# Optimization experiments

Measured on AMD Instinct MI355X. Metric: run time of the kernel, lower is better.

Reference implementation:

```python
import jax, jax.numpy as jnp
import numpy as np

NEG_SLOPE = 0.2
EPS = 1e-12


def setup_inputs() -> dict:
    key = jax.random.key(0)
    k1, k2, k3, k4, k5 = jax.random.split(key, 5)
    N, E, IN, OUT = 100000, 1600000, 256, 64
    x = jax.random.normal(k1, (N, IN), dtype=jnp.float32)
    edge_index = jax.random.randint(k2, (2, E), 0, N, dtype=jnp.int64)
    # GATConv (heads=1) parameters: lin weight, att_src, att_dst, bias
    W = jax.random.normal(k3, (IN, OUT), dtype=jnp.float32) * (1.0 / np.sqrt(IN))
    att_src = jax.random.normal(k4, (OUT,), dtype=jnp.float32) * (1.0 / np.sqrt(OUT))
    att_dst = jax.random.normal(k5, (OUT,), dtype=jnp.float32) * (1.0 / np.sqrt(OUT))
    bias = jnp.zeros((OUT,), dtype=jnp.float32)
    return {"x": x, "edge_index": edge_index, "W": W,
            "att_src": att_src, "att_dst": att_dst, "bias": bias}


def reference(x, edge_index, W, att_src, att_dst, bias):
    N = x.shape[0]
    # PyG GATConv default add_self_loops=True
    loops = jnp.arange(N, dtype=edge_index.dtype)
    src = jnp.concatenate([edge_index[0], loops])  # source j of edge (j -> i)
    dst = jnp.concatenate([edge_index[1], loops])  # target i (softmax segment)

    h = x @ W                                      # [N, out]
    a_src = h @ att_src                            # [N] per-node source score
    a_dst = h @ att_dst                            # [N] per-node target score

    e = jax.nn.leaky_relu(a_src[src] + a_dst[dst], NEG_SLOPE)  # [E+N]
    # segment softmax over incoming edges of each destination node
    e_max = jax.ops.segment_max(e, dst, num_segments=N)
    e = jnp.exp(e - e_max[dst])
    denom = jax.ops.segment_sum(e, dst, num_segments=N)
    alpha = e / denom[dst]                         # [E+N]

    # scatter-aggregate: out[i] = sum_j alpha_ij * h[j]
    out = jax.ops.segment_sum(alpha[:, None] * h[src], dst, num_segments=N)
    out = out + bias

    # dropout (p=0.3) in eval mode is identity; then F.normalize (row-wise L2)
    nrm = jnp.sqrt(jnp.sum(out * out, axis=-1, keepdims=True))
    return out / jnp.maximum(nrm, EPS)
```

## Files before the change

### kernel.cpp

```cpp
#include <hip/hip_runtime.h>
#include <hip/hip_bf16.h>
#include <math.h>

#define NEG_SLOPE 0.2f
#define EPS_NRM 1e-12f
#define K_IN 256
#define C_OUT 64
#define BK 32
#define TILE_M 64
#define XPAD 36

__global__ __launch_bounds__(256) void gemm_att(
    const float* __restrict__ x, const float* __restrict__ W,
    const float* __restrict__ att_s, const float* __restrict__ att_d,
    __hip_bfloat16* __restrict__ h, float* __restrict__ a_src_arr,
    float* __restrict__ a_dst_arr, int N,
    const int* __restrict__ dstA, int* __restrict__ cnt, int E)
{
    __shared__ float xs[2][TILE_M][XPAD];
    __shared__ float ws[2][BK][C_OUT];

    int t  = threadIdx.x;
    int tx = t & 15;
    int ty = t >> 4;
    int row0 = blockIdx.x * TILE_M;

    int xr  = t >> 2;
    int xko = (t & 3) * 8;
    int srow = row0 + xr; if (srow >= N) srow = N - 1;
    const float* xp = x + (size_t)srow * K_IN + xko;

    int wkr = t >> 3;
    int wco = (t & 7) * 8;
    const float* wp = W + (size_t)wkr * C_OUT + wco;

    float acc[4][4];
#pragma unroll
    for (int r = 0; r < 4; ++r)
#pragma unroll
        for (int c = 0; c < 4; ++c) acc[r][c] = 0.f;

    float4 xA = *(const float4*)(xp);
    float4 xB = *(const float4*)(xp + 4);
    float4 wA = *(const float4*)(wp);
    float4 wB = *(const float4*)(wp + 4);
    *(float4*)&xs[0][xr][xko]       = xA;
    *(float4*)&xs[0][xr][xko + 4]   = xB;
    *(float4*)&ws[0][wkr][wco]      = wA;
    *(float4*)&ws[0][wkr][wco + 4]  = wB;
    __syncthreads();

    int buf = 0;
    for (int k0 = 0; k0 < K_IN; k0 += BK) {
        const bool more = (k0 + BK) < K_IN;
        if (more) {
            xA = *(const float4*)(xp + k0 + BK);
            xB = *(const float4*)(xp + k0 + BK + 4);
            wA = *(const float4*)(wp + (size_t)(k0 + BK) * C_OUT);
            wB = *(const float4*)(wp + (size_t)(k0 + BK) * C_OUT + 4);
        }

#pragma unroll
        for (int kk = 0; kk < BK; kk += 4) {
            float xq[4][4];
            *(float4*)xq[0] = *(const float4*)&xs[buf][ty * 4 + 0][kk];
            *(float4*)xq[1] = *(const float4*)&xs[buf][ty * 4 + 1][kk];
            *(float4*)xq[2] = *(const float4*)&xs[buf][ty * 4 + 2][kk];
            *(float4*)xq[3] = *(const float4*)&xs[buf][ty * 4 + 3][kk];
#pragma unroll
            for (int j = 0; j < 4; ++j) {
                float4 wv = *(const float4*)&ws[buf][kk + j][tx * 4];
#pragma unroll
                for (int r = 0; r < 4; ++r) {
                    acc[r][0] += xq[r][j] * wv.x;
                    acc[r][1] += xq[r][j] * wv.y;
                    acc[r][2] += xq[r][j] * wv.z;
                    acc[r][3] += xq[r][j] * wv.w;
                }
            }
        }

        if (more) {
            *(float4*)&xs[buf ^ 1][xr][xko]      = xA;
            *(float4*)&xs[buf ^ 1][xr][xko + 4]  = xB;
            *(float4*)&ws[buf ^ 1][wkr][wco]     = wA;
            *(float4*)&ws[buf ^ 1][wkr][wco + 4] = wB;
            __syncthreads();
            buf ^= 1;
        }
    }

    float4 avl = *(const float4*)(att_s + tx * 4);
    float4 dvl = *(const float4*)(att_d + tx * 4);
#pragma unroll
    for (int r = 0; r < 4; ++r) {
        int row = row0 + ty * 4 + r;
        float ps = acc[r][0] * avl.x + acc[r][1] * avl.y +
                   acc[r][2] * avl.z + acc[r][3] * avl.w;
        float pd = acc[r][0] * dvl.x + acc[r][1] * dvl.y +
                   acc[r][2] * dvl.z + acc[r][3] * dvl.w;
#pragma unroll
        for (int d = 1; d < 16; d <<= 1) {
            ps += __shfl_xor(ps, d, 64);
            pd += __shfl_xor(pd, d, 64);
        }
        if (row < N) {
            if (tx == 0) { a_src_arr[row] = ps; a_dst_arr[row] = pd; }
            __hip_bfloat16 hb[4];
#pragma unroll
            for (int c = 0; c < 4; ++c) hb[c] = __float2bfloat16(acc[r][c]);
            *(ushort2*)(h + (size_t)row * C_OUT + tx * 4) =
                make_ushort2(*(unsigned short*)&hb[0], *(unsigned short*)&hb[1]);
            *(ushort2*)(h + (size_t)row * C_OUT + tx * 4 + 2) =
                make_ushort2(*(unsigned short*)&hb[2], *(unsigned short*)&hb[3]);
        }
    }

    int stride = gridDim.x * blockDim.x;
    for (int i = blockIdx.x * blockDim.x + t; i < E; i += stride)
        atomicAdd(&cnt[dstA[i]], 1);
}

__global__ __launch_bounds__(256) void scan_p1(
    const int* __restrict__ cnt, int* __restrict__ partials, int n)
{
    int b = blockIdx.x, t = threadIdx.x;
    int base = b * 1024;
    int s = 0;
#pragma unroll
    for (int j = 0; j < 4; ++j) {
        int i = base + t * 4 + j;
        if (i < n) s += cnt[i];
    }
    for (int d = 1; d < 64; d <<= 1) s += __shfl_xor(s, d, 64);
    __shared__ int wsum[4];
    int lane = t & 63, wid = t >> 6;
    if (lane == 0) wsum[wid] = s;
    __syncthreads();
    if (t == 0) partials[b] = wsum[0] + wsum[1] + wsum[2] + wsum[3];
}

__global__ __launch_bounds__(256) void scan_p2(int* partials, int nb)
{
    __shared__ int buf[256];
    int t = threadIdx.x;
    int v = (t < nb) ? partials[t] : 0;
    buf[t] = v;
    __syncthreads();
    for (int d = 1; d < 256; d <<= 1) {
        int w = (t >= d) ? buf[t - d] : 0;
        __syncthreads();
        buf[t] += w;
        __syncthreads();
    }
    if (t < nb) partials[t] = buf[t] - v;
}

__global__ __launch_bounds__(256) void scan_p3(
    const int* __restrict__ cnt, const int* __restrict__ partials,
    int* __restrict__ offsets, int n)
{
    int b = blockIdx.x, t = threadIdx.x;
    int base = b * 1024;
    int v[4];
    int s = 0;
#pragma unroll
    for (int j = 0; j < 4; ++j) {
        int i = base + t * 4 + j;
        v[j] = (i < n) ? cnt[i] : 0;
        s += v[j];
    }
    int lane = t & 63, wid = t >> 6;
    int incl = s;
    for (int d = 1; d < 64; d <<= 1) {
        int w = __shfl_up(incl, d, 64);
        if (lane >= d) incl += w;
    }
    __shared__ int wsum[4];
    __shared__ int wbase[4];
    if (lane == 63) wsum[wid] = incl;
    __syncthreads();
    if (t == 0) {
        int r = 0;
        for (int i = 0; i < 4; ++i) { wbase[i] = r; r += wsum[i]; }
    }
    __syncthreads();
    int run = partials[b] + wbase[wid] + (incl - s);
#pragma unroll
    for (int j = 0; j < 4; ++j) {
        int i = base + t * 4 + j;
        if (i < n) {
            offsets[i] = run;
            run += v[j];
            if (i == n - 1) offsets[n] = run;
        }
    }
}

__global__ __launch_bounds__(256) void scatter_edges(
    const int* __restrict__ srcA, const int* __restrict__ dstA,
    const int* __restrict__ offsets, int* __restrict__ cursor,
    const float* __restrict__ a_src, const float* __restrict__ a_dst,
    unsigned long long* __restrict__ csr, int E)
{
    int i = blockIdx.x * blockDim.x + threadIdx.x;
    if (i >= E) return;
    int s = srcA[i], d = dstA[i];
    float e = a_src[s] + a_dst[d];
    e = fmaxf(e, NEG_SLOPE * e);
    float w = __expf(e);
    int pos = offsets[d] + atomicAdd(&cursor[d], 1);
    unsigned long long packed =
        (unsigned long long)(unsigned)s |
        ((unsigned long long)__float_as_uint(w) << 32);
    __builtin_nontemporal_store(packed, &csr[pos]);
}

__global__ __launch_bounds__(256) void gat_pull(
    const int* __restrict__ offsets, const int2* __restrict__ csr,
    const unsigned short* __restrict__ h, const float* __restrict__ a_src,
    const float* __restrict__ a_dst, const float* __restrict__ bias,
    float* __restrict__ out, int N)
{
    int gw   = (blockIdx.x * blockDim.x + threadIdx.x) >> 6;
    int lane = threadIdx.x & 63;
    int grp  = lane >> 4;
    int gl   = lane & 15;
    int node = gw * 4 + grp;
    bool valid = node < N;
    int nv = valid ? node : 0;

    int beg = offsets[nv];
    int n   = valid ? (offsets[nv + 1] - beg) : 0;
    const int2* ce = csr + (n ? beg : 0);

    float asv = a_src[nv], adv = a_dst[nv];
    float es = asv + adv; es = fmaxf(es, NEG_SLOPE * es);
    float ws = __expf(es);
    unsigned long long hu = *(const unsigned long long*)
        (h + (size_t)nv * C_OUT + 4 * gl);
    unsigned hl = (unsigned)hu, hh = (unsigned)(hu >> 32);
    float acc0 = ws * __uint_as_float(hl << 16);
    float acc1 = ws * __uint_as_float(hl & 0xffff0000u);
    float acc2 = ws * __uint_as_float(hh << 16);
    float acc3 = ws * __uint_as_float(hh & 0xffff0000u);
    float den = ws;

    int2 c0 = ce[0];
    int2 c1 = ce[(n > 1) ? 1 : 0];
    unsigned long long u0 = *(const unsigned long long*)
        (h + (size_t)c0.x * C_OUT + 4 * gl);
    unsigned long long u1 = *(const unsigned long long*)
        (h + (size_t)c1.x * C_OUT + 4 * gl);

    for (int p = 0; p < n; p += 2) {
        int2 m0 = ce[(p + 2 < n) ? p + 2 : 0];
        int2 m1 = ce[(p + 3 < n) ? p + 3 : 0];
        unsigned long long v0 = *(const unsigned long long*)
            (h + (size_t)m0.x * C_OUT + 4 * gl);
        unsigned long long v1 = *(const unsigned long long*)
            (h + (size_t)m1.x * C_OUT + 4 * gl);

        float w0 = __int_as_float(c0.y);
        float w1 = (p + 1 < n) ? __int_as_float(c1.y) : 0.f;
        unsigned l0 = (unsigned)u0, h0 = (unsigned)(u0 >> 32);
        unsigned l1 = (unsigned)u1, h1 = (unsigned)(u1 >> 32);
        den  += w0 + w1;
        acc0 += w0 * __uint_as_float(l0 << 16)
              + w1 * __uint_as_float(l1 << 16);
        acc1 += w0 * __uint_as_float(l0 & 0xffff0000u)
              + w1 * __uint_as_float(l1 & 0xffff0000u);
        acc2 += w0 * __uint_as_float(h0 << 16)
              + w1 * __uint_as_float(h1 << 16);
        acc3 += w0 * __uint_as_float(h0 & 0xffff0000u)
              + w1 * __uint_as_float(h1 & 0xffff0000u);

        c0 = m0; c1 = m1; u0 = v0; u1 = v1;
    }

    float4 bl = *(const float4*)(bias + 4 * gl);
    float rd = 1.f / den;
    float o0 = acc0 * rd + bl.x;
    float o1 = acc1 * rd + bl.y;
    float o2 = acc2 * rd + bl.z;
    float o3 = acc3 * rd + bl.w;

    float sq = o0 * o0 + o1 * o1 + o2 * o2 + o3 * o3;
#pragma unroll
    for (int d = 1; d < 16; d <<= 1) sq += __shfl_xor(sq, d, 64);
    float rn = 1.f / fmaxf(sqrtf(sq), EPS_NRM);

    if (valid)
        *(float4*)(out + (size_t)node * C_OUT + 4 * gl) =
            make_float4(o0 * rn, o1 * rn, o2 * rn, o3 * rn);
}

extern "C" void kernel_launch(void* const* d_in, const int* in_sizes, int n_in,
                              void* d_out, int out_size, void* d_ws, size_t ws_size,
                              hipStream_t stream)
{
    const float* x     = (const float*)d_in[0];
    const int*   ei    = (const int*)d_in[1];
    const float* W     = (const float*)d_in[2];
    const float* att_s = (const float*)d_in[3];
    const float* att_d = (const float*)d_in[4];
    const float* bias  = (const float*)d_in[5];
    float*       out   = (float*)d_out;

    const int OUT = in_sizes[3];
    const int IN  = in_sizes[2] / OUT;
    const int N   = in_sizes[0] / IN;
    const int E   = in_sizes[1] / 2;

    char* w = (char*)d_ws;
    auto alloc = [&](size_t bytes) -> void* {
        void* p = (void*)w;
        w += (bytes + 255) & ~(size_t)255;
        return p;
    };
    __hip_bfloat16* h = (__hip_bfloat16*)alloc((size_t)N * C_OUT * 2);
    float* a_src  = (float*)alloc((size_t)N * 4);
    float* a_dst  = (float*)alloc((size_t)N * 4);
    int*   cnt    = (int*)alloc((size_t)N * 2 * 4);
    int*   offs   = (int*)alloc((size_t)(N + 1) * 4);
    int*   parts  = (int*)alloc(1024 * 4);
    unsigned long long* csr = (unsigned long long*)alloc((size_t)E * 8);
    int*   cursor = cnt + N;

    hipMemsetAsync(cnt, 0, (size_t)N * 2 * 4, stream);

    gemm_att<<<(N + TILE_M - 1) / TILE_M, 256, 0, stream>>>(
        x, W, att_s, att_d, h, a_src, a_dst, N, ei + E, cnt, E);

    int NB = (N + 1023) / 1024;
    scan_p1<<<NB, 256, 0, stream>>>(cnt, parts, N);
    scan_p2<<<1, 256, 0, stream>>>(parts, NB);
    scan_p3<<<NB, 256, 0, stream>>>(cnt, parts, offs, N);

    scatter_edges<<<(E + 255) / 256, 256, 0, stream>>>(
        ei, ei + E, offs, cursor, a_src, a_dst, csr, E);

    gat_pull<<<(N + 15) / 16, 256, 0, stream>>>(offs, (const int2*)csr,
        (const unsigned short*)h, a_src, a_dst, bias, out, N);
}
```

Baseline: 352.5 us.

## Single-buffer GEMM shared memory and raise occupancy hint in gemm_att

Replaces the double-buffered shared-memory tiles in the projection GEMM with single buffers, adding a second barrier per K-step, and sets launch_bounds min blocks to 8. The aim is to halve LDS use per block and raise occupancy so more waves hide global load latency. In exchange it adds a barrier per iteration and may force register limits that cause spills.

```diff
diff --git a/kernel.cpp b/kernel.cpp
--- a/kernel.cpp
+++ b/kernel.cpp
@@ -10,15 +10,15 @@
 #define TILE_M 64
 #define XPAD 36
 
-__global__ __launch_bounds__(256) void gemm_att(
+__global__ __launch_bounds__(256, 8) void gemm_att(
     const float* __restrict__ x, const float* __restrict__ W,
     const float* __restrict__ att_s, const float* __restrict__ att_d,
     __hip_bfloat16* __restrict__ h, float* __restrict__ a_src_arr,
     float* __restrict__ a_dst_arr, int N,
     const int* __restrict__ dstA, int* __restrict__ cnt, int E)
 {
-    __shared__ float xs[2][TILE_M][XPAD];
-    __shared__ float ws[2][BK][C_OUT];
+    __shared__ float xs[TILE_M][XPAD];
+    __shared__ float ws[BK][C_OUT];
 
     int t  = threadIdx.x;
     int tx = t & 15;
@@ -44,13 +44,12 @@
     float4 xB = *(const float4*)(xp + 4);
     float4 wA = *(const float4*)(wp);
     float4 wB = *(const float4*)(wp + 4);
-    *(float4*)&xs[0][xr][xko]       = xA;
-    *(float4*)&xs[0][xr][xko + 4]   = xB;
-    *(float4*)&ws[0][wkr][wco]      = wA;
-    *(float4*)&ws[0][wkr][wco + 4]  = wB;
-    __syncthreads();
-
-    int buf = 0;
+    *(float4*)&xs[xr][xko]      = xA;
+    *(float4*)&xs[xr][xko + 4]  = xB;
+    *(float4*)&ws[wkr][wco]     = wA;
+    *(float4*)&ws[wkr][wco + 4] = wB;
+    __syncthreads();
+
     for (int k0 = 0; k0 < K_IN; k0 += BK) {
         const bool more = (k0 + BK) < K_IN;
         if (more) {
@@ -63,13 +62,13 @@
 #pragma unroll
         for (int kk = 0; kk < BK; kk += 4) {
             float xq[4][4];
-            *(float4*)xq[0] = *(const float4*)&xs[buf][ty * 4 + 0][kk];
-            *(float4*)xq[1] = *(const float4*)&xs[buf][ty * 4 + 1][kk];
-            *(float4*)xq[2] = *(const float4*)&xs[buf][ty * 4 + 2][kk];
-            *(float4*)xq[3] = *(const float4*)&xs[buf][ty * 4 + 3][kk];
+            *(float4*)xq[0] = *(const float4*)&xs[ty * 4 + 0][kk];
+            *(float4*)xq[1] = *(const float4*)&xs[ty * 4 + 1][kk];
+            *(float4*)xq[2] = *(const float4*)&xs[ty * 4 + 2][kk];
+            *(float4*)xq[3] = *(const float4*)&xs[ty * 4 + 3][kk];
 #pragma unroll
             for (int j = 0; j < 4; ++j) {
-                float4 wv = *(const float4*)&ws[buf][kk + j][tx * 4];
+                float4 wv = *(const float4*)&ws[kk + j][tx * 4];
 #pragma unroll
                 for (int r = 0; r < 4; ++r) {
                     acc[r][0] += xq[r][j] * wv.x;
@@ -81,12 +80,12 @@
         }
 
         if (more) {
-            *(float4*)&xs[buf ^ 1][xr][xko]      = xA;
-            *(float4*)&xs[buf ^ 1][xr][xko + 4]  = xB;
-            *(float4*)&ws[buf ^ 1][wkr][wco]     = wA;
-            *(float4*)&ws[buf ^ 1][wkr][wco + 4] = wB;
             __syncthreads();
-            buf ^= 1;
+            *(float4*)&xs[xr][xko]      = xA;
+            *(float4*)&xs[xr][xko + 4]  = xB;
+            *(float4*)&ws[wkr][wco]     = wA;
+            *(float4*)&ws[wkr][wco + 4] = wB;
+            __syncthreads();
         }
     }
 
```

Result: slower. 448.7 us (+27.3%).
